# Kernel optimization log

Measured on AMD Instinct MI355X. Metric: run time of the kernel, lower is better.

The kernel has to match this reference:

```python
import jax, jax.numpy as jnp
import numpy as np

SEQ, BATCH, HIDDEN = 2048, 2, 1024
NUM_HEADS, HEAD_DIM = 16, 64
LN_EPS = 1e-6
NEG_INF = -1e10


def setup_inputs() -> dict:
    key = jax.random.key(0)
    k1, k2, k3 = jax.random.split(key, 3)
    inputs_q = jax.random.normal(k1, (SEQ, BATCH, HIDDEN), dtype=jnp.float32)
    ln_scale = jnp.ones((HIDDEN,), dtype=jnp.float32)
    ln_bias = jnp.zeros((HIDDEN,), dtype=jnp.float32)
    # fused QKV kernel: (hidden, 3, num_heads*head_dim), fan_in variance scaling
    qkv_kernel = jax.random.normal(k2, (HIDDEN, 3, NUM_HEADS * HEAD_DIM), dtype=jnp.float32) / np.sqrt(HIDDEN).astype(np.float32)
    out_kernel = jax.random.normal(k3, (NUM_HEADS * HEAD_DIM, HIDDEN), dtype=jnp.float32) / np.sqrt(NUM_HEADS * HEAD_DIM).astype(np.float32)
    return {"inputs_q": inputs_q, "ln_scale": ln_scale, "ln_bias": ln_bias,
            "qkv_kernel": qkv_kernel, "out_kernel": out_kernel}


def reference(inputs_q, ln_scale, ln_bias, qkv_kernel, out_kernel):
    s, b, h = inputs_q.shape
    # --- LayerNorm (fused with QKV projection in the original module) ---
    mu = jnp.mean(inputs_q, axis=-1, keepdims=True)
    var = jnp.mean(jnp.square(inputs_q - mu), axis=-1, keepdims=True)
    ln_out = (inputs_q - mu) * jax.lax.rsqrt(var + LN_EPS) * ln_scale + ln_bias
    # --- fused QKV projection: (s,b,h) @ (h,3,nh*hd) -> (s,b,3,nh*hd) ---
    qkv = jnp.einsum('sbh,htk->stbk', ln_out, qkv_kernel)  # (s,3,b,nh*hd)
    q = qkv[:, 0].reshape(s, b, NUM_HEADS, HEAD_DIM)  # (s,b,nh,hd)
    k = qkv[:, 1].reshape(s, b, NUM_HEADS, HEAD_DIM)
    v = qkv[:, 2].reshape(s, b, NUM_HEADS, HEAD_DIM)
    # --- core attention (transpose_batch_sequence=True layout) ---
    scale = 1.0 / np.sqrt(HEAD_DIM).astype(np.float32)  # scale_attn_logits=True
    logits = jnp.einsum('qbhd,kbhd->bhqk', q, k) * scale
    causal = jnp.tril(jnp.ones((s, s), dtype=bool))  # attn_mask_type='causal'
    logits = jnp.where(causal[None, None], logits, jnp.asarray(NEG_INF, logits.dtype))
    attn = jax.nn.softmax(logits, axis=-1)
    ctx = jnp.einsum('bhqk,kbhd->qbhd', attn, v).reshape(s, b, NUM_HEADS * HEAD_DIM)
    # --- output projection ---
    return jnp.einsum('sbk,kh->sbh', ctx, out_kernel)
```

## Files before the change

### kernel.cpp

```cpp
#include <hip/hip_runtime.h>

typedef unsigned short u16;
typedef unsigned int u32;
typedef __attribute__((ext_vector_type(8))) short short8;
typedef __attribute__((ext_vector_type(4))) float f32x4;

#define AS1C(p) ((const __attribute__((address_space(1))) void*)(p))
#define AS3(p)  ((__attribute__((address_space(3))) void*)(p))

constexpr int SEQ = 2048, BATCH = 2, HIDDEN = 1024, NH = 16, HD = 64;
constexpr int MROWS = SEQ * BATCH;
constexpr int QKV_N = 3 * NH * HD;
#define Q_SCALE 0.18033688011112042f

__device__ __forceinline__ float bf2f(u16 u) {
  union { u32 i; float f; } v; v.i = (u32)u << 16; return v.f;
}
__device__ __forceinline__ u16 f2bf(float f) {
  union { float f; u32 i; } v; v.f = f;
  u32 r = v.i + 0x7fffu + ((v.i >> 16) & 1u);
  return (u16)(r >> 16);
}
__device__ __forceinline__ u32 cvt_pk_bf16(float lo, float hi) {
  u32 r;
  asm("v_cvt_pk_bf16_f32 %0, %1, %2" : "=v"(r) : "v"(lo), "v"(hi));
  return r;
}
__device__ __forceinline__ bool is_f32(const unsigned* probe) { return probe[0] == 0x3F800000u; }

__global__ __launch_bounds__(256) void pre_k(const void* __restrict__ xv, const void* __restrict__ gv,
                                             const void* __restrict__ bv, u16* __restrict__ y,
                                             const void* __restrict__ wqkv, u16* __restrict__ qkvT,
                                             const void* __restrict__ wout, u16* __restrict__ outT,
                                             const unsigned* __restrict__ probe) {
  const bool fm = is_f32(probe);
  const int bid = blockIdx.x;
  if (bid < MROWS) {
    const int row = bid, t = threadIdx.x;
    float f0, f1, f2, f3, g0, g1, g2, g3, b0, b1, b2, b3;
    if (fm) {
      float4 v = *(const float4*)((const float*)xv + (size_t)row * HIDDEN + t * 4);
      f0 = v.x; f1 = v.y; f2 = v.z; f3 = v.w;
      float4 gg = *(const float4*)((const float*)gv + t * 4);
      g0 = gg.x; g1 = gg.y; g2 = gg.z; g3 = gg.w;
      float4 bb = *(const float4*)((const float*)bv + t * 4);
      b0 = bb.x; b1 = bb.y; b2 = bb.z; b3 = bb.w;
    } else {
      ushort4 v = *(const ushort4*)((const u16*)xv + (size_t)row * HIDDEN + t * 4);
      f0 = bf2f(v.x); f1 = bf2f(v.y); f2 = bf2f(v.z); f3 = bf2f(v.w);
      ushort4 gg = *(const ushort4*)((const u16*)gv + t * 4);
      g0 = bf2f(gg.x); g1 = bf2f(gg.y); g2 = bf2f(gg.z); g3 = bf2f(gg.w);
      ushort4 bb = *(const ushort4*)((const u16*)bv + t * 4);
      b0 = bf2f(bb.x); b1 = bf2f(bb.y); b2 = bf2f(bb.z); b3 = bf2f(bb.w);
    }
    float s = f0 + f1 + f2 + f3;
    float s2 = f0 * f0 + f1 * f1 + f2 * f2 + f3 * f3;
#pragma unroll
    for (int off = 1; off < 64; off <<= 1) { s += __shfl_xor(s, off); s2 += __shfl_xor(s2, off); }
    __shared__ float ps[4], ps2[4];
    int w = t >> 6, lane = t & 63;
    if (lane == 0) { ps[w] = s; ps2[w] = s2; }
    __syncthreads();
    s = ps[0] + ps[1] + ps[2] + ps[3];
    s2 = ps2[0] + ps2[1] + ps2[2] + ps2[3];
    float mu = s * (1.0f / HIDDEN);
    float rstd = rsqrtf(s2 * (1.0f / HIDDEN) - mu * mu + 1e-6f);
    ushort4 o;
    o.x = f2bf((f0 - mu) * rstd * g0 + b0);
    o.y = f2bf((f1 - mu) * rstd * g1 + b1);
    o.z = f2bf((f2 - mu) * rstd * g2 + b2);
    o.w = f2bf((f3 - mu) * rstd * g3 + b3);
    *(ushort4*)(y + (size_t)row * HIDDEN + t * 4) = o;
  } else {
    __shared__ alignas(16) u16 t[32][33];
    const int tb = bid - MROWS;
    const void* in;
    u16* out;
    int C, c0, r0;
    if (tb < 3072) { in = wqkv; out = qkvT; C = QKV_N; c0 = (tb % 96) * 32; r0 = (tb / 96) * 32; }
    else { const int t2 = tb - 3072; in = wout; out = outT; C = HIDDEN; c0 = (t2 & 31) * 32; r0 = (t2 >> 5) * 32; }
    int tx = threadIdx.x & 31, ty = threadIdx.x >> 5;
    if (fm) {
      const float* fin = (const float*)in;
#pragma unroll
      for (int i = 0; i < 32; i += 8) t[ty + i][tx] = f2bf(fin[(size_t)(r0 + ty + i) * C + c0 + tx]);
    } else {
      const u16* uin = (const u16*)in;
#pragma unroll
      for (int i = 0; i < 32; i += 8) t[ty + i][tx] = uin[(size_t)(r0 + ty + i) * C + c0 + tx];
    }
    __syncthreads();
#pragma unroll
    for (int i = 0; i < 32; i += 8) out[(size_t)(c0 + ty + i) * HIDDEN + r0 + tx] = t[tx][ty + i];
  }
}

template <int EPI>
__global__ __launch_bounds__(256) void gemm_k(const u16* __restrict__ A, const u16* __restrict__ Bt,
                                              void* __restrict__ o0, u16* __restrict__ o1,
                                              u16* __restrict__ o2, int M, int N, int K,
                                              const unsigned* __restrict__ probe) {
  __shared__ alignas(16) u16 As[2][128 * 32];
  __shared__ alignas(16) u16 Bs[2][128 * 32];
  const int bm = blockIdx.x, bn = blockIdx.y;
  const int tid = threadIdx.x, w = tid >> 6, lane = tid & 63;
  const int wr = w >> 1, wc = w & 1, lr = lane & 15, lk = lane >> 4;
  f32x4 acc[4][4] = {};

  const int srow_lo = lane >> 2;
  const int sslot = lane & 3;
  const int csw = ((lk ^ ((lr >> 1) & 3)) * 8);
  const int nk = K >> 5;

  int srowA[2], srcA[2];
#pragma unroll
  for (int j = 0; j < 2; j++) {
    const int issue = w * 2 + j;
    srowA[j] = issue * 16 + srow_lo;
    srcA[j] = ((sslot ^ ((srowA[j] >> 1) & 3)) * 8);
  }

#define STAGE(kt, bufi)                                                                     \
  {                                                                                         \
    const int k0s = (kt) * 32;                                                              \
    _Pragma("unroll")                                                                       \
    for (int j = 0; j < 2; j++) {                                                           \
      const int issue = w * 2 + j;                                                          \
      __builtin_amdgcn_global_load_lds(                                                     \
          AS1C(A + (size_t)(bm * 128 + srowA[j]) * K + k0s + srcA[j]),                      \
          AS3(As[bufi] + issue * 512 + lane * 8), 16, 0, 0);                                \
      __builtin_amdgcn_global_load_lds(                                                     \
          AS1C(Bt + (size_t)(bn * 128 + srowA[j]) * K + k0s + srcA[j]),                     \
          AS3(Bs[bufi] + issue * 512 + lane * 8), 16, 0, 0);                                \
    }                                                                                       \
  }

  STAGE(0, 0);
  __syncthreads();

  int buf = 0;
  for (int kt = 0; kt < nk; ++kt) {
    if (kt + 1 < nk) STAGE(kt + 1, buf ^ 1);
    short8 a[4], b[4];
#pragma unroll
    for (int i = 0; i < 4; i++) {
      a[i] = *(const short8*)(As[buf] + (wr * 64 + i * 16 + lr) * 32 + csw);
      b[i] = *(const short8*)(Bs[buf] + (wc * 64 + i * 16 + lr) * 32 + csw);
    }
#pragma unroll
    for (int mi = 0; mi < 4; mi++)
#pragma unroll
      for (int ni = 0; ni < 4; ni++)
        acc[mi][ni] = __builtin_amdgcn_mfma_f32_16x16x32_bf16(a[mi], b[ni], acc[mi][ni], 0, 0, 0);
    __syncthreads();
    buf ^= 1;
  }
#undef STAGE

  const int r0 = bm * 128 + wr * 64, c0 = bn * 128 + wc * 64;
  if constexpr (EPI == 0) {
    const bool fm = is_f32(probe);
#pragma unroll
    for (int mi = 0; mi < 4; mi++)
#pragma unroll
      for (int ni = 0; ni < 4; ni++) {
        int col = c0 + ni * 16 + lr;
#pragma unroll
        for (int j = 0; j < 4; j++) {
          int row = r0 + mi * 16 + lk * 4 + j;
          if (fm) ((float*)o0)[(size_t)row * N + col] = acc[mi][ni][j];
          else    ((u16*)o0)[(size_t)row * N + col] = f2bf(acc[mi][ni][j]);
        }
      }
  } else {
#pragma unroll
    for (int mi = 0; mi < 4; mi++)
#pragma unroll
      for (int ni = 0; ni < 4; ni++) {
        int n = c0 + ni * 16 + lr;
        int t = n >> 10, rem = n & 1023, h = rem >> 6, d = rem & 63;
#pragma unroll
        for (int j = 0; j < 4; j++) {
          int r = r0 + mi * 16 + lk * 4 + j;
          int s = r >> 1, bb = r & 1;
          size_t bh = (size_t)(bb * NH + h);
          if (t == 0)      ((u16*)o0)[(bh * SEQ + s) * HD + d] = f2bf(acc[mi][ni][j] * Q_SCALE);
          else if (t == 1) o1[(bh * SEQ + s) * HD + d] = f2bf(acc[mi][ni][j]);
          else             o2[(bh * HD + d) * SEQ + s] = f2bf(acc[mi][ni][j]);
        }
      }
  }
}

__global__ __launch_bounds__(256, 4) void attn_k(const u16* __restrict__ Q, const u16* __restrict__ Kb,
                                                 const u16* __restrict__ VT, u16* __restrict__ ctx) {
  const int flat = blockIdx.x;
  const int xu = flat & 7, idx = flat >> 3;
  const int bh = xu * 4 + (idx & 3);
  const int qt = 31 - (idx >> 2);
  const int tid = threadIdx.x;
  const int w = tid >> 6, lane = tid & 63;
  const int lr = lane & 15, lk = lane >> 4;
  const size_t base = (size_t)bh * SEQ * HD;
  const int b = bh >> 4, h = bh & 15;

  __shared__ alignas(16) u16 Ks[2][4096];
  __shared__ alignas(16) u16 Vs[2][4096];
  __shared__ alignas(16) u16 P[4][16 * 64];
  u16* Pw = &P[w][0];
  u32* Pw32 = (u32*)Pw;

  const int st_r = lane >> 3;
  const int st_c = 8 * ((lane & 7) ^ st_r);
  const int swz = (lr & 7) << 3;
  const int psw = (lr & 7) << 1;

  const int qr0 = qt * 64 + w * 16;
  const int qrow = qr0 + lr;
  const int klast = qt;

  short8 aq[2];
#pragma unroll
  for (int kk = 0; kk < 2; kk++)
    aq[kk] = *(const short8*)(Q + base + (size_t)qrow * HD + kk * 32 + lk * 8);

  f32x4 o[4] = {};
  float l = 0.0f;

#pragma unroll
  for (int j2 = 0; j2 < 2; j2++) {
    const int c = j2 * 4 + w;
    const int r = c * 8 + st_r;
    __builtin_amdgcn_global_load_lds(AS1C(Kb + base + (size_t)r * HD + st_c),
                                     AS3(Ks[0] + c * 512), 16, 0, 0);
    __builtin_amdgcn_global_load_lds(AS1C(VT + base + (size_t)r * SEQ + st_c),
                                     AS3(Vs[0] + c * 512), 16, 0, 0);
  }
  __syncthreads();

  for (int kt = 0; kt <= klast; kt++) {
    const int k0 = kt * 64;
    const int buf = kt & 1;
    if (kt < klast) {
      const int kn = k0 + 64;
#pragma unroll
      for (int j2 = 0; j2 < 2; j2++) {
        const int c = j2 * 4 + w;
        const int r = c * 8 + st_r;
        __builtin_amdgcn_global_load_lds(AS1C(Kb + base + (size_t)(kn + r) * HD + st_c),
                                         AS3(Ks[buf ^ 1] + c * 512), 16, 0, 0);
        __builtin_amdgcn_global_load_lds(AS1C(VT + base + (size_t)r * SEQ + kn + st_c),
                                         AS3(Vs[buf ^ 1] + c * 512), 16, 0, 0);
      }
    }
    short8 bk[4][2], bv[4][2];
#pragma unroll
    for (int ni = 0; ni < 4; ni++) {
      const int row = ni * 16 + lr;
#pragma unroll
      for (int kk = 0; kk < 2; kk++)
        bk[ni][kk] = *(const short8*)(Ks[buf] + row * 64 + ((kk * 32 + lk * 8) ^ swz));
#pragma unroll
      for (int ks = 0; ks < 2; ks++)
        bv[ni][ks] = *(const short8*)(Vs[buf] + row * 64 + ((ks * 32 + lk * 8) ^ swz));
    }
    f32x4 s[4] = {};
#pragma unroll
    for (int ni = 0; ni < 4; ni++)
#pragma unroll
      for (int kk = 0; kk < 2; kk++)
        s[ni] = __builtin_amdgcn_mfma_f32_16x16x32_bf16(bk[ni][kk], aq[kk], s[ni], 0, 0, 0);
    if (kt == klast) {
#pragma unroll
      for (int ni = 0; ni < 4; ni++)
#pragma unroll
        for (int jj = 0; jj < 4; jj++)
          if (k0 + ni * 16 + lk * 4 + jj > qrow) s[ni][jj] = -1e30f;
    }
#pragma unroll
    for (int ni = 0; ni < 4; ni++) {
#pragma unroll
      for (int jj = 0; jj < 4; jj++) s[ni][jj] = exp2f(s[ni][jj]);
      l += (s[ni][0] + s[ni][1]) + (s[ni][2] + s[ni][3]);
    }
#pragma unroll
    for (int ni = 0; ni < 4; ni++) {
      uint2 pk;
      pk.x = cvt_pk_bf16(s[ni][0], s[ni][1]);
      pk.y = cvt_pk_bf16(s[ni][2], s[ni][3]);
      *(uint2*)(Pw32 + lr * 32 + 2 * ((4 * ni + lk) ^ psw)) = pk;
    }
    short8 pa[2];
#pragma unroll
    for (int kk = 0; kk < 2; kk++)
      pa[kk] = *(const short8*)(Pw + lr * 64 + 4 * (((kk << 3) + (lk << 1)) ^ psw));
#pragma unroll
    for (int ni = 0; ni < 4; ni++)
#pragma unroll
      for (int kk = 0; kk < 2; kk++)
        o[ni] = __builtin_amdgcn_mfma_f32_16x16x32_bf16(pa[kk], bv[ni][kk], o[ni], 0, 0, 0);
    __syncthreads();
  }
  float lf = l;
  lf += __shfl_xor(lf, 16);
  lf += __shfl_xor(lf, 32);
  float linv0 = 1.0f / __shfl(lf, lk * 4 + 0);
  float linv1 = 1.0f / __shfl(lf, lk * 4 + 1);
  float linv2 = 1.0f / __shfl(lf, lk * 4 + 2);
  float linv3 = 1.0f / __shfl(lf, lk * 4 + 3);
#pragma unroll
  for (int ni = 0; ni < 4; ni++) {
    int col = h * HD + ni * 16 + lr;
    ctx[(size_t)((qr0 + lk * 4 + 0) * BATCH + b) * (NH * HD) + col] = f2bf(o[ni][0] * linv0);
    ctx[(size_t)((qr0 + lk * 4 + 1) * BATCH + b) * (NH * HD) + col] = f2bf(o[ni][1] * linv1);
    ctx[(size_t)((qr0 + lk * 4 + 2) * BATCH + b) * (NH * HD) + col] = f2bf(o[ni][2] * linv2);
    ctx[(size_t)((qr0 + lk * 4 + 3) * BATCH + b) * (NH * HD) + col] = f2bf(o[ni][3] * linv3);
  }
}

extern "C" void kernel_launch(void* const* d_in, const int* in_sizes, int n_in,
                              void* d_out, int out_size, void* d_ws, size_t ws_size,
                              hipStream_t stream) {
  const void* x    = d_in[0];
  const void* g    = d_in[1];
  const void* bta  = d_in[2];
  const void* wqkv = d_in[3];
  const void* wout = d_in[4];
  const unsigned* probe = (const unsigned*)d_in[1];

  char* ws = (char*)d_ws;
  u16* ln   = (u16*)(ws);
  u16* q    = (u16*)(ws + 8388608);
  u16* k    = (u16*)(ws + 16777216);
  u16* vT   = (u16*)(ws + 25165824);
  u16* qkvT = (u16*)(ws + 33554432);
  u16* outT = (u16*)(ws + 33554432 + 6291456);
  u16* ctx  = ln;

  pre_k<<<dim3(MROWS + 3072 + 1024), 256, 0, stream>>>(x, g, bta, ln, wqkv, qkvT, wout, outT, probe);
  gemm_k<1><<<dim3(MROWS / 128, QKV_N / 128), 256, 0, stream>>>(ln, qkvT, q, k, vT,
                                                                MROWS, QKV_N, HIDDEN, probe);
  attn_k<<<dim3(1024), 256, 0, stream>>>(q, k, vT, ctx);
  gemm_k<0><<<dim3(MROWS / 128, HIDDEN / 128), 256, 0, stream>>>(ctx, outT, d_out, nullptr,
                                                                 nullptr, MROWS, HIDDEN,
                                                                 HIDDEN, probe);
}
```

Measured before the change: 110.6 us.

## Use 256x256 tiled 8-wave GEMM with 4-stage LDS pipeline for QKV projection

Replaces the 128x128 QKV projection GEMM with a new 512-thread kernel that computes 256x256 output tiles. Each K step is split into interleaved halves, with direct global-to-LDS loads, explicit vmcnt waits and raw barriers so loads overlap MFMA work, and setprio raised around the MFMA blocks. The larger tile is meant to raise operand reuse and cut memory traffic per FLOP. In exchange the grid shrinks to 16x12 = 192 blocks, which may leave some compute units idle, and the hand-written synchronisation is more fragile.

```diff
diff --git a/kernel.cpp b/kernel.cpp
--- a/kernel.cpp
+++ b/kernel.cpp
@@ -27,6 +27,11 @@
   return r;
 }
 __device__ __forceinline__ bool is_f32(const unsigned* probe) { return probe[0] == 0x3F800000u; }
+
+__device__ __forceinline__ void barrier_raw() {
+  __builtin_amdgcn_s_barrier();
+  __builtin_amdgcn_sched_barrier(0);
+}
 
 __global__ __launch_bounds__(256) void pre_k(const void* __restrict__ xv, const void* __restrict__ gv,
                                              const void* __restrict__ bv, u16* __restrict__ y,
@@ -95,10 +100,131 @@
   }
 }
 
-template <int EPI>
+__global__ __launch_bounds__(512, 2) void gemm256_k(const u16* __restrict__ A, const u16* __restrict__ Bt,
+                                                    u16* __restrict__ qO, u16* __restrict__ kO,
+                                                    u16* __restrict__ vO, int K) {
+  __shared__ alignas(16) u16 LA[4][8192];
+  __shared__ alignas(16) u16 LB[4][8192];
+  const int bm = blockIdx.x, bn = blockIdx.y;
+  const int tid = threadIdx.x, w = tid >> 6, lane = tid & 63;
+  const int wm = w >> 2, wn = w & 3;
+  const int lr = lane & 15, lk = lane >> 4;
+  const int csw = 8 * (lk ^ ((lr >> 1) & 3));
+  const int srow = tid >> 2;
+  const int scol = 8 * ((tid & 3) ^ ((srow >> 1) & 3));
+
+  f32x4 acc[8][4] = {};
+  const int nIter = K >> 6;
+
+#define G2L(src, dst) __builtin_amdgcn_global_load_lds(AS1C(src), AS3(dst), 16, 0, 0)
+#define STAGE_A(t_, s_)                                                           \
+  { const u16* sp = A + (size_t)(bm * 256 + srow) * K + (t_) * 32 + scol;         \
+    G2L(sp, LA[s_] + tid * 8);                                                    \
+    G2L(sp + (size_t)128 * K, LA[s_] + tid * 8 + 4096); }
+#define STAGE_B(t_, s_)                                                           \
+  { const u16* sp = Bt + (size_t)(bn * 256 + srow) * K + (t_) * 32 + scol;        \
+    G2L(sp, LB[s_] + tid * 8);                                                    \
+    G2L(sp + (size_t)128 * K, LB[s_] + tid * 8 + 4096); }
+
+  STAGE_A(0, 0); STAGE_B(0, 0); STAGE_A(1, 1); STAGE_B(1, 1);
+  asm volatile("s_waitcnt vmcnt(4)" ::: "memory");
+  barrier_raw();
+
+  short8 bfr[4], afr[4];
+#pragma unroll 1
+  for (int j = 0; j < nIter; ++j) {
+    const int s0 = (j & 1) << 1, s1 = s0 + 1;
+    const int d0 = s0 ^ 2, d1 = s1 ^ 2;
+    const int t0 = 2 * j, t1 = 2 * j + 1;
+    const bool st = (j < nIter - 1);
+#pragma unroll
+    for (int ni = 0; ni < 4; ni++)
+      bfr[ni] = *(const short8*)(LB[s0] + (wn * 64 + ni * 16 + lr) * 32 + csw);
+#pragma unroll
+    for (int m = 0; m < 4; m++)
+      afr[m] = *(const short8*)(LA[s0] + (wm * 128 + m * 16 + lr) * 32 + csw);
+    if (st) STAGE_A(t0 + 2, d0);
+    barrier_raw();
+    __builtin_amdgcn_s_setprio(1);
+#pragma unroll
+    for (int m = 0; m < 4; m++)
+#pragma unroll
+      for (int ni = 0; ni < 4; ni++)
+        acc[m][ni] = __builtin_amdgcn_mfma_f32_16x16x32_bf16(afr[m], bfr[ni], acc[m][ni], 0, 0, 0);
+    __builtin_amdgcn_s_setprio(0);
+    barrier_raw();
+#pragma unroll
+    for (int m = 0; m < 4; m++)
+      afr[m] = *(const short8*)(LA[s0] + (wm * 128 + (m + 4) * 16 + lr) * 32 + csw);
+    if (st) STAGE_B(t0 + 2, d0);
+    barrier_raw();
+    __builtin_amdgcn_s_setprio(1);
+#pragma unroll
+    for (int m = 0; m < 4; m++)
+#pragma unroll
+      for (int ni = 0; ni < 4; ni++)
+        acc[m + 4][ni] = __builtin_amdgcn_mfma_f32_16x16x32_bf16(afr[m], bfr[ni], acc[m + 4][ni], 0, 0, 0);
+    __builtin_amdgcn_s_setprio(0);
+    if (st) { asm volatile("s_waitcnt vmcnt(4)" ::: "memory"); }
+    else    { asm volatile("s_waitcnt vmcnt(0)" ::: "memory"); }
+    __builtin_amdgcn_sched_barrier(0);
+    barrier_raw();
+#pragma unroll
+    for (int ni = 0; ni < 4; ni++)
+      bfr[ni] = *(const short8*)(LB[s1] + (wn * 64 + ni * 16 + lr) * 32 + csw);
+#pragma unroll
+    for (int m = 0; m < 4; m++)
+      afr[m] = *(const short8*)(LA[s1] + (wm * 128 + m * 16 + lr) * 32 + csw);
+    if (st) STAGE_A(t1 + 2, d1);
+    barrier_raw();
+    __builtin_amdgcn_s_setprio(1);
+#pragma unroll
+    for (int m = 0; m < 4; m++)
+#pragma unroll
+      for (int ni = 0; ni < 4; ni++)
+        acc[m][ni] = __builtin_amdgcn_mfma_f32_16x16x32_bf16(afr[m], bfr[ni], acc[m][ni], 0, 0, 0);
+    __builtin_amdgcn_s_setprio(0);
+    barrier_raw();
+#pragma unroll
+    for (int m = 0; m < 4; m++)
+      afr[m] = *(const short8*)(LA[s1] + (wm * 128 + (m + 4) * 16 + lr) * 32 + csw);
+    if (st) STAGE_B(t1 + 2, d1);
+    barrier_raw();
+    __builtin_amdgcn_s_setprio(1);
+#pragma unroll
+    for (int m = 0; m < 4; m++)
+#pragma unroll
+      for (int ni = 0; ni < 4; ni++)
+        acc[m + 4][ni] = __builtin_amdgcn_mfma_f32_16x16x32_bf16(afr[m], bfr[ni], acc[m + 4][ni], 0, 0, 0);
+    __builtin_amdgcn_s_setprio(0);
+    if (st) { asm volatile("s_waitcnt vmcnt(4)" ::: "memory"); __builtin_amdgcn_sched_barrier(0); }
+    barrier_raw();
+  }
+#undef STAGE_A
+#undef STAGE_B
+#undef G2L
+
+  const int r0 = bm * 256 + wm * 128, c0 = bn * 256 + wn * 64;
+#pragma unroll
+  for (int mi = 0; mi < 8; mi++)
+#pragma unroll
+    for (int ni = 0; ni < 4; ni++) {
+      int n = c0 + ni * 16 + lr;
+      int t = n >> 10, rem = n & 1023, h = rem >> 6, d = rem & 63;
+#pragma unroll
+      for (int jj = 0; jj < 4; jj++) {
+        int r = r0 + mi * 16 + lk * 4 + jj;
+        int s = r >> 1, bb = r & 1;
+        size_t bh = (size_t)(bb * NH + h);
+        if (t == 0)      qO[(bh * SEQ + s) * HD + d] = f2bf(acc[mi][ni][jj] * Q_SCALE);
+        else if (t == 1) kO[(bh * SEQ + s) * HD + d] = f2bf(acc[mi][ni][jj]);
+        else             vO[(bh * HD + d) * SEQ + s] = f2bf(acc[mi][ni][jj]);
+      }
+    }
+}
+
 __global__ __launch_bounds__(256) void gemm_k(const u16* __restrict__ A, const u16* __restrict__ Bt,
-                                              void* __restrict__ o0, u16* __restrict__ o1,
-                                              u16* __restrict__ o2, int M, int N, int K,
+                                              void* __restrict__ o0, int M, int N, int K,
                                               const unsigned* __restrict__ probe) {
   __shared__ alignas(16) u16 As[2][128 * 32];
   __shared__ alignas(16) u16 Bs[2][128 * 32];
@@ -158,38 +284,19 @@
 #undef STAGE
 
   const int r0 = bm * 128 + wr * 64, c0 = bn * 128 + wc * 64;
-  if constexpr (EPI == 0) {
-    const bool fm = is_f32(probe);
-#pragma unroll
-    for (int mi = 0; mi < 4; mi++)
-#pragma unroll
-      for (int ni = 0; ni < 4; ni++) {
-        int col = c0 + ni * 16 + lr;
-#pragma unroll
-        for (int j = 0; j < 4; j++) {
-          int row = r0 + mi * 16 + lk * 4 + j;
-          if (fm) ((float*)o0)[(size_t)row * N + col] = acc[mi][ni][j];
-          else    ((u16*)o0)[(size_t)row * N + col] = f2bf(acc[mi][ni][j]);
-        }
+  const bool fm = is_f32(probe);
+#pragma unroll
+  for (int mi = 0; mi < 4; mi++)
+#pragma unroll
+    for (int ni = 0; ni < 4; ni++) {
+      int col = c0 + ni * 16 + lr;
+#pragma unroll
+      for (int j = 0; j < 4; j++) {
+        int row = r0 + mi * 16 + lk * 4 + j;
+        if (fm) ((float*)o0)[(size_t)row * N + col] = acc[mi][ni][j];
+        else    ((u16*)o0)[(size_t)row * N + col] = f2bf(acc[mi][ni][j]);
       }
-  } else {
-#pragma unroll
-    for (int mi = 0; mi < 4; mi++)
-#pragma unroll
-      for (int ni = 0; ni < 4; ni++) {
-        int n = c0 + ni * 16 + lr;
-        int t = n >> 10, rem = n & 1023, h = rem >> 6, d = rem & 63;
-#pragma unroll
-        for (int j = 0; j < 4; j++) {
-          int r = r0 + mi * 16 + lk * 4 + j;
-          int s = r >> 1, bb = r & 1;
-          size_t bh = (size_t)(bb * NH + h);
-          if (t == 0)      ((u16*)o0)[(bh * SEQ + s) * HD + d] = f2bf(acc[mi][ni][j] * Q_SCALE);
-          else if (t == 1) o1[(bh * SEQ + s) * HD + d] = f2bf(acc[mi][ni][j]);
-          else             o2[(bh * HD + d) * SEQ + s] = f2bf(acc[mi][ni][j]);
-        }
-      }
-  }
+    }
 }
 
 __global__ __launch_bounds__(256, 4) void attn_k(const u16* __restrict__ Q, const u16* __restrict__ Kb,
@@ -338,10 +445,8 @@
   u16* ctx  = ln;
 
   pre_k<<<dim3(MROWS + 3072 + 1024), 256, 0, stream>>>(x, g, bta, ln, wqkv, qkvT, wout, outT, probe);
-  gemm_k<1><<<dim3(MROWS / 128, QKV_N / 128), 256, 0, stream>>>(ln, qkvT, q, k, vT,
-                                                                MROWS, QKV_N, HIDDEN, probe);
+  gemm256_k<<<dim3(MROWS / 256, QKV_N / 256), 512, 0, stream>>>(ln, qkvT, q, k, vT, HIDDEN);
   attn_k<<<dim3(1024), 256, 0, stream>>>(q, k, vT, ctx);
-  gemm_k<0><<<dim3(MROWS / 128, HIDDEN / 128), 256, 0, stream>>>(ctx, outT, d_out, nullptr,
-                                                                 nullptr, MROWS, HIDDEN,
-                                                                 HIDDEN, probe);
-}
+  gemm_k<<<dim3(MROWS / 128, HIDDEN / 128), 256, 0, stream>>>(ctx, outT, d_out,
+                                                              MROWS, HIDDEN, HIDDEN, probe);
+}
```

Result: slower. 131.6 us (+19.0%).
